# Kernel tuning notes

Hardware: AMD Instinct MI355X
Metric: run time of the kernel (lower is better)

The kernel has to match this reference:

```python
import jax, jax.numpy as jnp
import numpy as np

VOCAB = 32000
EMB = 1024
SEQ = 2048
STACK = 8
N_HEADS = 16
ATTN = 64
BATCH = 2


def _ln(x, g, b, eps=1e-5):
    mu = jnp.mean(x, axis=-1, keepdims=True)
    var = jnp.var(x, axis=-1, keepdims=True)
    return (x - mu) * jax.lax.rsqrt(var + eps) * g + b


def setup_inputs() -> dict:
    key = jax.random.key(0)
    ks = jax.random.split(key, 16)
    s = lambda *sh: 0.02
    inp = {
        "x": jax.random.randint(ks[0], (BATCH, SEQ), 0, VOCAB),
        "emb": jax.random.normal(ks[1], (VOCAB, EMB), jnp.float32) * 0.02,
        # NOTE: one shared Attention_Head (all n_heads identical) and one shared Decoder (all stack layers identical)
        "Wq": jax.random.normal(ks[2], (EMB, ATTN), jnp.float32) * 0.02,
        "bq": jnp.zeros((ATTN,), jnp.float32),
        "Wk": jax.random.normal(ks[3], (EMB, ATTN), jnp.float32) * 0.02,
        "bk": jnp.zeros((ATTN,), jnp.float32),
        "Wv": jax.random.normal(ks[4], (EMB, ATTN), jnp.float32) * 0.02,
        "bv": jnp.zeros((ATTN,), jnp.float32),
        "Wd": jax.random.normal(ks[5], (ATTN * N_HEADS, EMB), jnp.float32) * 0.02,
        "bd": jnp.zeros((EMB,), jnp.float32),
        "g1": jnp.ones((EMB,), jnp.float32),
        "beta1": jnp.zeros((EMB,), jnp.float32),
        "g2": jnp.ones((EMB,), jnp.float32),
        "beta2": jnp.zeros((EMB,), jnp.float32),
        "W1": jax.random.normal(ks[6], (EMB, 4 * EMB), jnp.float32) * 0.02,
        "c1": jnp.zeros((4 * EMB,), jnp.float32),
        "W2": jax.random.normal(ks[7], (4 * EMB, EMB), jnp.float32) * 0.02,
        "c2": jnp.zeros((EMB,), jnp.float32),
        "Wfc": jax.random.normal(ks[8], (EMB, VOCAB), jnp.float32) * 0.02,
        "bfc": jnp.zeros((VOCAB,), jnp.float32),
    }
    return inp


def reference(x, emb, Wq, bq, Wk, bk, Wv, bv, Wd, bd, g1, beta1, g2, beta2, W1, c1, W2, c2, Wfc, bfc):
    h = emb[x]  # [B, S, E]
    scale = ATTN ** (-0.5)
    for _ in range(STACK):  # same (shared) decoder params every layer
        z = _ln(h, g1, beta1)
        q = z @ Wq + bq  # [B,S,A]
        k = z @ Wk + bk
        v = z @ Wv + bv
        # no causal mask applied in the original (tril buffer is unused)
        attn = jax.nn.softmax(jnp.einsum("bqa,bka->bqk", q, k) * scale, axis=-1)
        head = attn @ v  # [B,S,A]; all heads share weights -> identical outputs
        cat = jnp.tile(head, (1, 1, N_HEADS))  # [B,S,A*H]
        h = h + cat @ Wd + bd
        z2 = _ln(h, g2, beta2)
        h = h + jax.nn.relu(z2 @ W1 + c1) @ W2 + c2
    return h @ Wfc + bfc  # [B,S,VOCAB]
```

## Files before the change

kernel.cpp:

```cpp
#include <hip/hip_runtime.h>

typedef unsigned short u16;
typedef __attribute__((ext_vector_type(4))) float f32x4;
typedef __attribute__((ext_vector_type(8))) __bf16 bf16x8;
typedef __attribute__((ext_vector_type(4))) unsigned short u16x4;

static __device__ __forceinline__ u16 f2bf(float f) {
  union { float f; unsigned u; } v; v.f = f;
  unsigned r = v.u + 0x7fffu + ((v.u >> 16) & 1u);
  return (u16)(r >> 16);
}

#define GLD_LDS(g, l) __builtin_amdgcn_global_load_lds( \
    (const __attribute__((address_space(1))) void*)(g), \
    (__attribute__((address_space(3))) void*)(l), 16, 0, 0)

template<int EPI>
__global__ __launch_bounds__(512, 2)
void gemm8p(const u16* __restrict__ A, const u16* __restrict__ B,
            float* __restrict__ Cf, u16* __restrict__ Cb,
            const float* __restrict__ bias, float alpha,
            int K, int lda, int ldb, int ldc, int mtiles, int gm, int nsplit,
            long long sA, long long sB, long long sC)
{
  extern __shared__ u16 lds8[];
  const int t = threadIdx.x;
  const int w = t >> 6, l = t & 63;
  const int l15 = l & 15, l16 = l >> 4;
  const int wr = w >> 2, wc = w & 3;

  int wg = blockIdx.x;
  const int nwg = gridDim.x;
  {
    const int q = nwg >> 3, r = nwg & 7;
    const int xcd = wg & 7, loc = wg >> 3;
    wg = (xcd < r ? xcd * (q + 1) : r * (q + 1) + (xcd - r) * q) + loc;
  }
  const int ntiles = nwg / mtiles;
  const int gsz = gm * ntiles;
  const int gi = wg / gsz;
  const int rr = wg - gi * gsz;
  const int nt = rr / gm;
  const int mt = gi * gm + (rr - nt * gm);
  const int m0 = mt << 8, n0 = nt << 8;

  const int bz = blockIdx.z;
  int batch = bz, sp = 0;
  if (nsplit > 1) { batch = bz / nsplit; sp = bz - batch * nsplit; }
  const u16* Ab = A + (long long)batch * sA + (long long)sp * K;
  const u16* Bb = B + (long long)batch * sB + (long long)sp * K;
  const long long cbase = (long long)bz * sC;

  const int srow = t >> 3;
  const int scol = (((t & 7) ^ (srow & 7)) << 3);
  const u16* gA[4]; const u16* gB[4];
#pragma unroll
  for (int i = 0; i < 4; ++i) {
    gA[i] = Ab + (long long)(m0 + i * 64 + srow) * lda + scol;
    gB[i] = Bb + (long long)(n0 + i * 64 + srow) * ldb + scol;
  }
  const int ldst = w << 9;

  auto STAGE = [&](int buf) {
#pragma unroll
    for (int i = 0; i < 4; ++i) {
      GLD_LDS(gA[i], &lds8[buf * 16384 + i * 4096 + ldst]);
      gA[i] += 64;
    }
#pragma unroll
    for (int i = 0; i < 4; ++i) {
      GLD_LDS(gB[i], &lds8[32768 + buf * 16384 + i * 4096 + ldst]);
      gB[i] += 64;
    }
  };

  STAGE(0);
  STAGE(1);

  f32x4 acc[8][4] = {};
  const int nkt = K >> 6;
  const int aRow = wr * 128 + l15;
  const int bRow = wc * 64 + l15;
  const int swz = l15 & 7;

  for (int kt = 0; kt < nkt; ++kt) {
    const int buf = kt & 1;
    if (kt < nkt - 1) asm volatile("s_waitcnt vmcnt(8)" ::: "memory");
    else              asm volatile("s_waitcnt vmcnt(0)" ::: "memory");
    __builtin_amdgcn_s_barrier();
    __builtin_amdgcn_sched_barrier(0);

    const int abase = buf * 16384;
    const int bbase = 32768 + buf * 16384;
    bf16x8 af[4][2], bf[4][2];
#pragma unroll
    for (int mf = 0; mf < 4; ++mf)
#pragma unroll
      for (int kk = 0; kk < 2; ++kk)
        af[mf][kk] = *(const bf16x8*)&lds8[abase + (aRow + mf * 16) * 64 + ((((kk << 2) + l16)) ^ swz) * 8];
#pragma unroll
    for (int nf = 0; nf < 4; ++nf)
#pragma unroll
      for (int kk = 0; kk < 2; ++kk)
        bf[nf][kk] = *(const bf16x8*)&lds8[bbase + (bRow + nf * 16) * 64 + ((((kk << 2) + l16)) ^ swz) * 8];

    __builtin_amdgcn_s_setprio(1);
#pragma unroll
    for (int mf = 0; mf < 4; ++mf)
#pragma unroll
      for (int nf = 0; nf < 4; ++nf)
#pragma unroll
        for (int kk = 0; kk < 2; ++kk)
          acc[mf][nf] = __builtin_amdgcn_mfma_f32_16x16x32_bf16(af[mf][kk], bf[nf][kk], acc[mf][nf], 0, 0, 0);
    __builtin_amdgcn_s_setprio(0);

    bf16x8 ah[4][2];
#pragma unroll
    for (int mf = 0; mf < 4; ++mf)
#pragma unroll
      for (int kk = 0; kk < 2; ++kk)
        ah[mf][kk] = *(const bf16x8*)&lds8[abase + (aRow + 64 + mf * 16) * 64 + ((((kk << 2) + l16)) ^ swz) * 8];

    asm volatile("s_waitcnt lgkmcnt(0)" ::: "memory");
    __builtin_amdgcn_s_barrier();
    __builtin_amdgcn_sched_barrier(0);
    if (kt + 2 < nkt) STAGE(buf);

    __builtin_amdgcn_s_setprio(1);
#pragma unroll
    for (int mf = 0; mf < 4; ++mf)
#pragma unroll
      for (int nf = 0; nf < 4; ++nf)
#pragma unroll
        for (int kk = 0; kk < 2; ++kk)
          acc[mf + 4][nf] = __builtin_amdgcn_mfma_f32_16x16x32_bf16(ah[mf][kk], bf[nf][kk], acc[mf + 4][nf], 0, 0, 0);
    __builtin_amdgcn_s_setprio(0);
  }

#pragma unroll
  for (int mf = 0; mf < 8; ++mf) {
    const int rbase = m0 + wr * 128 + mf * 16 + l16 * 4;
#pragma unroll
    for (int nf = 0; nf < 4; ++nf) {
      const int col = n0 + wc * 64 + nf * 16 + l15;
      const float bv = bias ? bias[col] : 0.f;
#pragma unroll
      for (int r = 0; r < 4; ++r) {
        const long long idx = cbase + (long long)(rbase + r) * ldc + col;
        const float v = acc[mf][nf][r];
        if (EPI == 0)      Cf[idx] = alpha * v + bv;
        else if (EPI == 2) Cb[idx] = f2bf(v + bv);
        else               { float x = v + bv; Cb[idx] = f2bf(x > 0.f ? x : 0.f); }
      }
    }
  }
}

template<int EPI>
__global__ __launch_bounds__(256)
void gemm_bt(const u16* __restrict__ A, const u16* __restrict__ B,
             float* __restrict__ Cf, u16* __restrict__ Cb,
             const float* __restrict__ bias, float alpha,
             int K, int lda, int ldb, int ldc, int mtiles, int gm, int nsplit,
             long long sA, long long sB, long long sC)
{
  __shared__ u16 ldsA[128 * 32];
  __shared__ u16 ldsB[128 * 32];
  const int t = threadIdx.x;
  const int w = t >> 6, l = t & 63;

  int wg = blockIdx.x;
  const int nwg = gridDim.x;
  {
    const int q = nwg >> 3, r = nwg & 7;
    const int xcd = wg & 7, loc = wg >> 3;
    wg = (xcd < r ? xcd * (q + 1) : r * (q + 1) + (xcd - r) * q) + loc;
  }
  const int ntiles = nwg / mtiles;
  const int gsz = gm * ntiles;
  const int gi = wg / gsz;
  const int rr = wg - gi * gsz;
  const int nt = rr / gm;
  const int mt = gi * gm + (rr - nt * gm);
  const int m0 = mt << 7, n0 = nt << 7;

  const int bzRaw = blockIdx.z;
  int batch = bzRaw, sp = 0;
  if (nsplit > 1) { batch = bzRaw / nsplit; sp = bzRaw - batch * nsplit; }
  const u16* Ab = A + (long long)batch * sA + (long long)sp * K;
  const u16* Bb = B + (long long)batch * sB + (long long)sp * K;
  const long long cbase = (long long)bzRaw * sC;

  const int wr = (w >> 1) << 6, wc = (w & 1) << 6;
  const int l15 = l & 15, l16 = l >> 4;
  f32x4 acc[4][4] = {};

  for (int k0 = 0; k0 < K; k0 += 32) {
#pragma unroll
    for (int r = 0; r < 2; ++r) {
      const int o = (r << 12) + (t << 4);
      const int row = o >> 6;
      const int cole = (o & 63) >> 1;
      GLD_LDS(Ab + (long long)(m0 + row) * lda + k0 + cole, &ldsA[(r << 11) + (w << 9)]);
      GLD_LDS(Bb + (long long)(n0 + row) * ldb + k0 + cole, &ldsB[(r << 11) + (w << 9)]);
    }
    __syncthreads();
    bf16x8 af[4], bg[4];
#pragma unroll
    for (int i = 0; i < 4; ++i) {
      af[i] = *(const bf16x8*)&ldsA[(wr + i * 16 + l15) * 32 + l16 * 8];
      bg[i] = *(const bf16x8*)&ldsB[(wc + i * 16 + l15) * 32 + l16 * 8];
    }
#pragma unroll
    for (int i = 0; i < 4; ++i)
#pragma unroll
      for (int j = 0; j < 4; ++j)
        acc[i][j] = __builtin_amdgcn_mfma_f32_16x16x32_bf16(af[i], bg[j], acc[i][j], 0, 0, 0);
    __syncthreads();
  }

#pragma unroll
  for (int i = 0; i < 4; ++i) {
    const int rbase = m0 + wr + i * 16 + l16 * 4;
#pragma unroll
    for (int j = 0; j < 4; ++j) {
      const int col = n0 + wc + j * 16 + l15;
      const float bv = bias ? bias[col] : 0.f;
#pragma unroll
      for (int r = 0; r < 4; ++r) {
        const long long idx = cbase + (long long)(rbase + r) * ldc + col;
        const float v = acc[i][j][r];
        if (EPI == 0)      Cf[idx] = alpha * v + bv;
        else if (EPI == 1) Cf[idx] += v + bv;
        else if (EPI == 2) Cb[idx] = f2bf(v + bv);
        else               { float x = v + bv; Cb[idx] = f2bf(x > 0.f ? x : 0.f); }
      }
    }
  }
}

__device__ __forceinline__ void fstep(
    const bf16x8 (&ck)[4][2], const bf16x8 (&cv)[4][2],
    bf16x8 (&nk)[4][2], bf16x8 (&nv)[4][2],
    const bf16x8 (&qf)[2], float (&m)[4], float (&ls)[4], f32x4 (&o)[4],
    const u16* qb, const u16* vb, int kv0, int kvn, u16* pl, int l15, int l16)
{
  f32x4 s[4] = {};
#pragma unroll
  for (int ni = 0; ni < 4; ++ni)
#pragma unroll
    for (int kk = 0; kk < 2; ++kk)
      s[ni] = __builtin_amdgcn_mfma_f32_16x16x32_bf16(qf[kk], ck[ni][kk], s[ni], 0, 0, 0);
#pragma unroll
  for (int ni = 0; ni < 4; ++ni)
#pragma unroll
    for (int kk = 0; kk < 2; ++kk)
      nk[ni][kk] = *(const bf16x8*)(qb + (kvn + ni * 16 + l15) * 256 + 64 + kk * 32 + l16 * 8);
#pragma unroll
  for (int ni = 0; ni < 4; ++ni) s[ni] *= 0.125f;
  float al[4], ps[4];
#pragma unroll
  for (int r = 0; r < 4; ++r) {
    float v = fmaxf(fmaxf(s[0][r], s[1][r]), fmaxf(s[2][r], s[3][r]));
    v = fmaxf(v, __shfl_xor(v, 1)); v = fmaxf(v, __shfl_xor(v, 2));
    v = fmaxf(v, __shfl_xor(v, 4)); v = fmaxf(v, __shfl_xor(v, 8));
    const float mn = fmaxf(m[r], v);
    al[r] = __expf(m[r] - mn);
    m[r] = mn;
    ps[r] = 0.f;
  }
#pragma unroll
  for (int ni = 0; ni < 4; ++ni)
#pragma unroll
    for (int r = 0; r < 4; ++r) {
      const float p = __expf(s[ni][r] - m[r]);
      ps[r] += p;
      pl[(l16 * 4 + r) * 72 + ni * 16 + l15] = f2bf(p);
    }
#pragma unroll
  for (int r = 0; r < 4; ++r) {
    float t = ps[r];
    t += __shfl_xor(t, 1); t += __shfl_xor(t, 2);
    t += __shfl_xor(t, 4); t += __shfl_xor(t, 8);
    ls[r] = ls[r] * al[r] + t;
  }
#pragma unroll
  for (int nd = 0; nd < 4; ++nd)
#pragma unroll
    for (int r = 0; r < 4; ++r) o[nd][r] *= al[r];
  bf16x8 pa[2];
#pragma unroll
  for (int kk = 0; kk < 2; ++kk)
    pa[kk] = *(const bf16x8*)&pl[l15 * 72 + kk * 32 + l16 * 8];
#pragma unroll
  for (int nd = 0; nd < 4; ++nd)
#pragma unroll
    for (int kk = 0; kk < 2; ++kk)
      o[nd] = __builtin_amdgcn_mfma_f32_16x16x32_bf16(pa[kk], cv[nd][kk], o[nd], 0, 0, 0);
#pragma unroll
  for (int nd = 0; nd < 4; ++nd)
#pragma unroll
    for (int kk = 0; kk < 2; ++kk)
      nv[nd][kk] = *(const bf16x8*)(vb + (nd * 16 + l15) * 2048 + kvn + kk * 32 + l16 * 8);
  (void)kv0;
}

__global__ __launch_bounds__(64)
void flash_k(const u16* __restrict__ qkv, const u16* __restrict__ vT,
             u16* __restrict__ head)
{
  __shared__ u16 pl[16 * 72];
  const int l = threadIdx.x, l15 = l & 15, l16 = l >> 4;
  const int b = blockIdx.x >> 7, q0 = (blockIdx.x & 127) << 4;
  const u16* qb = qkv + (long long)b * 2048 * 256;
  const u16* vb = vT + (long long)b * 64 * 2048;
  bf16x8 qf[2];
#pragma unroll
  for (int kk = 0; kk < 2; ++kk)
    qf[kk] = *(const bf16x8*)(qb + (q0 + l15) * 256 + kk * 32 + l16 * 8);
  float m[4], ls[4];
  f32x4 o[4] = {};
#pragma unroll
  for (int r = 0; r < 4; ++r) { m[r] = -1e30f; ls[r] = 0.f; }
  bf16x8 ka[4][2], va[4][2], kb[4][2], vb2[4][2];
#pragma unroll
  for (int ni = 0; ni < 4; ++ni)
#pragma unroll
    for (int kk = 0; kk < 2; ++kk) {
      ka[ni][kk] = *(const bf16x8*)(qb + (ni * 16 + l15) * 256 + 64 + kk * 32 + l16 * 8);
      va[ni][kk] = *(const bf16x8*)(vb + (ni * 16 + l15) * 2048 + kk * 32 + l16 * 8);
    }
  for (int t = 0; t < 32; t += 2) {
    fstep(ka, va, kb, vb2, qf, m, ls, o, qb, vb, t * 64, (t + 1) * 64, pl, l15, l16);
    fstep(kb, vb2, ka, va, qf, m, ls, o, qb, vb, (t + 1) * 64,
          (t + 2 < 32 ? (t + 2) * 64 : 31 * 64), pl, l15, l16);
  }
#pragma unroll
  for (int nd = 0; nd < 4; ++nd)
#pragma unroll
    for (int r = 0; r < 4; ++r)
      head[((long long)b * 2048 + q0 + l16 * 4 + r) * 64 + nd * 16 + l15] =
          f2bf(o[nd][r] / ls[r]);
}

__global__ __launch_bounds__(256)
void ln_k(const float* __restrict__ x, const float* __restrict__ g,
          const float* __restrict__ b, u16* __restrict__ z)
{
  const long long row = blockIdx.x;
  f32x4 v = ((const f32x4*)(x + row * 1024))[threadIdx.x];
  float s = v[0] + v[1] + v[2] + v[3];
  float q = v[0] * v[0] + v[1] * v[1] + v[2] * v[2] + v[3] * v[3];
#pragma unroll
  for (int o = 32; o; o >>= 1) { s += __shfl_down(s, o); q += __shfl_down(q, o); }
  __shared__ float rs_[4], rq_[4];
  const int l = threadIdx.x & 63, w = threadIdx.x >> 6;
  if (l == 0) { rs_[w] = s; rq_[w] = q; }
  __syncthreads();
  s = rs_[0] + rs_[1] + rs_[2] + rs_[3];
  q = rq_[0] + rq_[1] + rq_[2] + rq_[3];
  const float mu = s * (1.f / 1024.f);
  const float rstd = rsqrtf(q * (1.f / 1024.f) - mu * mu + 1e-5f);
  const f32x4 gv = ((const f32x4*)g)[threadIdx.x];
  const f32x4 bv = ((const f32x4*)b)[threadIdx.x];
  u16x4 o4;
#pragma unroll
  for (int e = 0; e < 4; ++e) o4[e] = f2bf((v[e] - mu) * rstd * gv[e] + bv[e]);
  ((u16x4*)(z + row * 1024))[threadIdx.x] = o4;
}

template<int MODE>
__global__ __launch_bounds__(256)
void reduce_ln_k(const u16* __restrict__ p, float* __restrict__ h,
                 const float* __restrict__ c2, const float* __restrict__ g,
                 const float* __restrict__ b, u16* __restrict__ z)
{
  const long long row = blockIdx.x;
  const int t = threadIdx.x;
  const long long i4 = (row << 8) + t;
  f32x4 v = ((const f32x4*)h)[i4] + ((const f32x4*)c2)[t];
#pragma unroll
  for (int s = 0; s < 4; ++s) {
    u16x4 pv = ((const u16x4*)p)[i4 + (long long)s * 1048576];
#pragma unroll
    for (int e = 0; e < 4; ++e) {
      union { unsigned u; float f; } x; x.u = ((unsigned)pv[e]) << 16;
      v[e] += x.f;
    }
  }
  u16x4 o4;
  if (MODE == 1) {
#pragma unroll
    for (int e = 0; e < 4; ++e) o4[e] = f2bf(v[e]);
  } else {
    ((f32x4*)h)[i4] = v;
    float s = v[0] + v[1] + v[2] + v[3];
    float q = v[0] * v[0] + v[1] * v[1] + v[2] * v[2] + v[3] * v[3];
#pragma unroll
    for (int o = 32; o; o >>= 1) { s += __shfl_down(s, o); q += __shfl_down(q, o); }
    __shared__ float rs_[4], rq_[4];
    const int l = t & 63, w = t >> 6;
    if (l == 0) { rs_[w] = s; rq_[w] = q; }
    __syncthreads();
    s = rs_[0] + rs_[1] + rs_[2] + rs_[3];
    q = rq_[0] + rq_[1] + rq_[2] + rq_[3];
    const float mu = s * (1.f / 1024.f);
    const float rstd = rsqrtf(q * (1.f / 1024.f) - mu * mu + 1e-5f);
    const f32x4 gv = ((const f32x4*)g)[t];
    const f32x4 bv = ((const f32x4*)b)[t];
#pragma unroll
    for (int e = 0; e < 4; ++e) o4[e] = f2bf((v[e] - mu) * rstd * gv[e] + bv[e]);
  }
  ((u16x4*)z)[i4] = o4;
}

__global__ __launch_bounds__(256)
void gather_k(const int* __restrict__ x, const float* __restrict__ emb, float* __restrict__ h)
{
  const long long tok = blockIdx.x;
  const long long r = (long long)x[tok] << 8;
  ((f32x4*)h)[(tok << 8) + threadIdx.x] = ((const f32x4*)emb)[r + threadIdx.x];
}

__global__ __launch_bounds__(256)
void tcast_k(const float* __restrict__ in, u16* __restrict__ out, int R, int C)
{
  __shared__ float tile[32][33];
  const int tx = threadIdx.x & 31, ty = threadIdx.x >> 5;
  const long long r0 = (long long)blockIdx.y << 5, c0 = (long long)blockIdx.x << 5;
#pragma unroll
  for (int yy = 0; yy < 32; yy += 8)
    tile[ty + yy][tx] = in[(r0 + ty + yy) * C + c0 + tx];
  __syncthreads();
#pragma unroll
  for (int yy = 0; yy < 32; yy += 8)
    out[(c0 + ty + yy) * R + r0 + tx] = f2bf(tile[tx][ty + yy]);
}

__global__ __launch_bounds__(256)
void wqkv_k(const float* __restrict__ Wq, const float* __restrict__ Wk,
            const float* __restrict__ Wv, u16* __restrict__ o)
{
  const int n = blockIdx.y;
  const long long e = (long long)blockIdx.x * 256 + threadIdx.x;
  float v = 0.f;
  if (n < 64)       v = Wq[e * 64 + n];
  else if (n < 128) v = Wk[e * 64 + (n - 64)];
  else if (n < 192) v = Wv[e * 64 + (n - 128)];
  o[(long long)n * 1024 + e] = f2bf(v);
}

__global__ __launch_bounds__(256)
void bqkv_k(const float* __restrict__ bq, const float* __restrict__ bk,
            const float* __restrict__ bv, float* __restrict__ o)
{
  const int n = threadIdx.x;
  float v = 0.f;
  if (n < 64)       v = bq[n];
  else if (n < 128) v = bk[n - 64];
  else if (n < 192) v = bv[n - 128];
  o[n] = v;
}

__global__ __launch_bounds__(256)
void wdsum_k(const float* __restrict__ Wd, u16* __restrict__ o)
{
  const int i = blockIdx.x * 256 + threadIdx.x;
  const int a = i & 63, e = i >> 6;
  float s = 0.f;
#pragma unroll
  for (int hh = 0; hh < 16; ++hh) s += Wd[(long long)(hh * 64 + a) * 1024 + e];
  o[i] = f2bf(s);
}

__global__ __launch_bounds__(256)
void reduce_qkv(const float* __restrict__ p, const float* __restrict__ bqkv,
                u16* __restrict__ qkv, u16* __restrict__ vT)
{
  const long long i4 = (long long)blockIdx.x * 256 + threadIdx.x;
  const int c4 = (int)(i4 & 63);
  const long long row = i4 >> 6;
  f32x4 s = ((const f32x4*)p)[i4] + ((const f32x4*)p)[i4 + 262144]
          + ((const f32x4*)bqkv)[c4];
  u16x4 o;
#pragma unroll
  for (int e = 0; e < 4; ++e) o[e] = f2bf(s[e]);
  ((u16x4*)qkv)[i4] = o;
  if (c4 >= 32 && c4 < 48) {
    const long long b = row >> 11, sidx = row & 2047;
#pragma unroll
    for (int e = 0; e < 4; ++e) {
      const int a = (c4 - 32) * 4 + e;
      vT[(b * 64 + a) * 2048 + sidx] = o[e];
    }
  }
}

extern "C" void kernel_launch(void* const* d_in, const int* in_sizes, int n_in,
                              void* d_out, int out_size, void* d_ws, size_t ws_size,
                              hipStream_t stream) {
  const int*   x   = (const int*)d_in[0];
  const float* emb = (const float*)d_in[1];
  const float* Wq  = (const float*)d_in[2];
  const float* bq  = (const float*)d_in[3];
  const float* Wk  = (const float*)d_in[4];
  const float* bk  = (const float*)d_in[5];
  const float* Wv  = (const float*)d_in[6];
  const float* bv  = (const float*)d_in[7];
  const float* Wd  = (const float*)d_in[8];
  const float* bd  = (const float*)d_in[9];
  const float* g1  = (const float*)d_in[10];
  const float* be1 = (const float*)d_in[11];
  const float* g2  = (const float*)d_in[12];
  const float* be2 = (const float*)d_in[13];
  const float* W1  = (const float*)d_in[14];
  const float* c1  = (const float*)d_in[15];
  const float* W2  = (const float*)d_in[16];
  const float* c2  = (const float*)d_in[17];
  const float* Wfc = (const float*)d_in[18];
  const float* bfc = (const float*)d_in[19];
  float* out = (float*)d_out;

  hipFuncSetAttribute(reinterpret_cast<const void*>(gemm8p<0>),
                      hipFuncAttributeMaxDynamicSharedMemorySize, 131072);
  hipFuncSetAttribute(reinterpret_cast<const void*>(gemm8p<2>),
                      hipFuncAttributeMaxDynamicSharedMemorySize, 131072);
  hipFuncSetAttribute(reinterpret_cast<const void*>(gemm8p<3>),
                      hipFuncAttributeMaxDynamicSharedMemorySize, 131072);

  char* ws = (char*)d_ws;
  size_t off = 0;
  auto alloc = [&](size_t bytes) { void* p = ws + off; off = (off + bytes + 255) & ~(size_t)255; return p; };
  float*  h     = (float*) alloc(4096ull * 1024 * 4);
  u16*    z     = (u16*)   alloc(4096ull * 1024 * 2);
  u16*    qkv   = (u16*)   alloc(4096ull * 256 * 2);
  u16*    vT    = (u16*)   alloc(2ull * 64 * 2048 * 2);
  u16*    head  = (u16*)   alloc(4096ull * 64 * 2);
  u16*    mid   = (u16*)   alloc(4096ull * 4096 * 2);
  char*   SCR   = (char*)  alloc(2ull * 4096 * 1024 * 4);
  float*  partQ = (float*)SCR;
  u16*    partF = (u16*)SCR;
  u16*    Wqkvt = (u16*)   alloc(256ull * 1024 * 2);
  float*  bqkv  = (float*) alloc(256 * 4);
  u16*    Wdst  = (u16*)   alloc(1024ull * 64 * 2);
  u16*    W1t   = (u16*)   alloc(4096ull * 1024 * 2);
  u16*    W2t   = (u16*)   alloc(1024ull * 4096 * 2);
  u16*    Wfct  = (u16*)   alloc(32000ull * 1024 * 2);

  gather_k<<<4096, 256, 0, stream>>>(x, emb, h);
  wqkv_k<<<dim3(4, 256), 256, 0, stream>>>(Wq, Wk, Wv, Wqkvt);
  bqkv_k<<<1, 256, 0, stream>>>(bq, bk, bv, bqkv);
  wdsum_k<<<256, 256, 0, stream>>>(Wd, Wdst);
  tcast_k<<<dim3(128, 32), 256, 0, stream>>>(W1, W1t, 1024, 4096);
  tcast_k<<<dim3(32, 128), 256, 0, stream>>>(W2, W2t, 4096, 1024);
  tcast_k<<<dim3(1000, 32), 256, 0, stream>>>(Wfc, Wfct, 1024, 32000);

  for (int layer = 0; layer < 8; ++layer) {
    if (layer == 0)
      ln_k<<<4096, 256, 0, stream>>>(h, g1, be1, z);
    gemm_bt<0><<<dim3(64, 1, 2), 256, 0, stream>>>(z, Wqkvt, partQ, nullptr, nullptr, 1.f,
        512, 1024, 1024, 256, 32, 32, 2, 0, 0, 1048576);
    reduce_qkv<<<1024, 256, 0, stream>>>(partQ, bqkv, qkv, vT);
    flash_k<<<256, 64, 0, stream>>>(qkv, vT, head);
    gemm_bt<1><<<dim3(256, 1, 1), 256, 0, stream>>>(head, Wdst, h, nullptr, bd, 1.f,
        64, 64, 64, 1024, 32, 32, 1, 0, 0, 0);
    ln_k<<<4096, 256, 0, stream>>>(h, g2, be2, z);
    gemm8p<3><<<dim3(256, 1, 1), 512, 131072, stream>>>(z, W1t, nullptr, mid, c1, 1.f,
        1024, 1024, 1024, 4096, 16, 16, 1, 0, 0, 0);
    gemm8p<2><<<dim3(64, 1, 4), 512, 131072, stream>>>(mid, W2t, nullptr, partF, nullptr, 1.f,
        1024, 4096, 4096, 1024, 16, 16, 4, 0, 0, 4194304);
    if (layer < 7)
      reduce_ln_k<0><<<4096, 256, 0, stream>>>(partF, h, c2, g1, be1, z);
    else
      reduce_ln_k<1><<<4096, 256, 0, stream>>>(partF, h, c2, nullptr, nullptr, z);
  }
  gemm8p<0><<<dim3(2000, 1, 1), 512, 131072, stream>>>(z, Wfct, out, nullptr, bfc, 1.f,
      1024, 1024, 1024, 32000, 16, 8, 1, 0, 0, 0);
}
```

Measured before the change: 1.759 ms.

## Restructure GEMM main loop into four interleaved phases with split A/B staging

Rewrites the bf16 MFMA GEMM mainloop so each k-tile is processed in four quarter phases, each reading a subset of A/B fragments from LDS and issuing part of the next tile's global-to-LDS loads between MFMA bursts. A is staged one tile ahead and B two tiles ahead, in half-tile chunks with a new per-thread load layout. The goal is to hide global load latency and LDS reads behind MFMA work more evenly. In exchange it adds more barriers per iteration, which may cost synchronisation overhead.

```diff
diff --git a/kernel.cpp b/kernel.cpp
--- a/kernel.cpp
+++ b/kernel.cpp
@@ -14,6 +14,11 @@
 #define GLD_LDS(g, l) __builtin_amdgcn_global_load_lds( \
     (const __attribute__((address_space(1))) void*)(g), \
     (__attribute__((address_space(3))) void*)(l), 16, 0, 0)
+
+#define LGKM0() asm volatile("s_waitcnt lgkmcnt(0)" ::: "memory")
+#define SBAR() do { __builtin_amdgcn_sched_barrier(0); \
+                    __builtin_amdgcn_s_barrier(); \
+                    __builtin_amdgcn_sched_barrier(0); } while (0)
 
 template<int EPI>
 __global__ __launch_bounds__(512, 2)
@@ -51,91 +56,107 @@
   const u16* Bb = B + (long long)batch * sB + (long long)sp * K;
   const long long cbase = (long long)bz * sC;
 
-  const int srow = t >> 3;
-  const int scol = (((t & 7) ^ (srow & 7)) << 3);
-  const u16* gA[4]; const u16* gB[4];
-#pragma unroll
-  for (int i = 0; i < 4; ++i) {
-    gA[i] = Ab + (long long)(m0 + i * 64 + srow) * lda + scol;
-    gB[i] = Bb + (long long)(n0 + i * 64 + srow) * ldb + scol;
-  }
-  const int ldst = w << 9;
-
-  auto STAGE = [&](int buf) {
-#pragma unroll
-    for (int i = 0; i < 4; ++i) {
-      GLD_LDS(gA[i], &lds8[buf * 16384 + i * 4096 + ldst]);
-      gA[i] += 64;
-    }
-#pragma unroll
-    for (int i = 0; i < 4; ++i) {
-      GLD_LDS(gB[i], &lds8[32768 + buf * 16384 + i * 4096 + ldst]);
-      gB[i] += 64;
-    }
+  int srow[2], scol[2], sdst[2];
+#pragma unroll
+  for (int j = 0; j < 2; ++j) {
+    const int u = (j << 9) + (w << 6) + l;
+    srow[j] = u >> 3;
+    scol[j] = ((u & 7) ^ ((u >> 3) & 7)) << 3;
+    sdst[j] = ((j << 9) + (w << 6)) << 3;
+  }
+
+  auto STAGE_A = [&](int buf, int h, int ktgt) {
+#pragma unroll
+    for (int j = 0; j < 2; ++j)
+      GLD_LDS(Ab + (long long)(m0 + h * 128 + srow[j]) * lda + ktgt * 64 + scol[j],
+              &lds8[(buf * 2 + h) * 8192 + sdst[j]]);
   };
-
-  STAGE(0);
-  STAGE(1);
-
+  auto STAGE_B = [&](int buf, int h, int ktgt) {
+#pragma unroll
+    for (int j = 0; j < 2; ++j)
+      GLD_LDS(Bb + (long long)(n0 + h * 128 + srow[j]) * ldb + ktgt * 64 + scol[j],
+              &lds8[32768 + (buf * 2 + h) * 8192 + sdst[j]]);
+  };
+
+  bf16x8 aF[4][2], bF0[2][2], bF1[2][2];
   f32x4 acc[8][4] = {};
+
+  auto RDA = [&](int buf, int mbase) {
+#pragma unroll
+    for (int mf = 0; mf < 4; ++mf) {
+      const int r2 = (mbase + mf) * 16 + l15;
+#pragma unroll
+      for (int kk = 0; kk < 2; ++kk)
+        aF[mf][kk] = *(const bf16x8*)&lds8[(buf * 2 + wr) * 8192 + r2 * 64 +
+                                           (((kk << 2) + l16) ^ (r2 & 7)) * 8];
+    }
+  };
+  auto RDB = [&](bf16x8 (&dst)[2][2], int buf, int nbase) {
+#pragma unroll
+    for (int nf = 0; nf < 2; ++nf) {
+      const int r2 = (wc & 1) * 64 + (nbase + nf) * 16 + l15;
+#pragma unroll
+      for (int kk = 0; kk < 2; ++kk)
+        dst[nf][kk] = *(const bf16x8*)&lds8[32768 + (buf * 2 + (wc >> 1)) * 8192 + r2 * 64 +
+                                            (((kk << 2) + l16) ^ (r2 & 7)) * 8];
+    }
+  };
+
+#define MM16(MB, NB, BF) \
+  do { \
+    __builtin_amdgcn_s_setprio(1); \
+    _Pragma("unroll") \
+    for (int mf = 0; mf < 4; ++mf) \
+      _Pragma("unroll") \
+      for (int nf = 0; nf < 2; ++nf) \
+        _Pragma("unroll") \
+        for (int kk = 0; kk < 2; ++kk) \
+          acc[MB + mf][NB + nf] = __builtin_amdgcn_mfma_f32_16x16x32_bf16( \
+              aF[mf][kk], BF[nf][kk], acc[MB + mf][NB + nf], 0, 0, 0); \
+    __builtin_amdgcn_s_setprio(0); \
+  } while (0)
+
   const int nkt = K >> 6;
-  const int aRow = wr * 128 + l15;
-  const int bRow = wc * 64 + l15;
-  const int swz = l15 & 7;
+
+  STAGE_B(0, 0, 0); STAGE_B(0, 1, 0);
+  STAGE_A(0, 0, 0); STAGE_A(0, 1, 0);
+  if (1 < nkt) { STAGE_B(1, 0, 1); STAGE_B(1, 1, 1); }
+  asm volatile("s_waitcnt vmcnt(4)" ::: "memory");
+  SBAR();
 
   for (int kt = 0; kt < nkt; ++kt) {
-    const int buf = kt & 1;
-    if (kt < nkt - 1) asm volatile("s_waitcnt vmcnt(8)" ::: "memory");
-    else              asm volatile("s_waitcnt vmcnt(0)" ::: "memory");
-    __builtin_amdgcn_s_barrier();
+    const int buf = kt & 1, nb = buf ^ 1;
+    RDA(buf, 0); RDB(bF0, buf, 0);
+    if (kt + 1 < nkt) STAGE_A(nb, 0, kt + 1);
+    SBAR();
+    LGKM0();
     __builtin_amdgcn_sched_barrier(0);
-
-    const int abase = buf * 16384;
-    const int bbase = 32768 + buf * 16384;
-    bf16x8 af[4][2], bf[4][2];
-#pragma unroll
-    for (int mf = 0; mf < 4; ++mf)
-#pragma unroll
-      for (int kk = 0; kk < 2; ++kk)
-        af[mf][kk] = *(const bf16x8*)&lds8[abase + (aRow + mf * 16) * 64 + ((((kk << 2) + l16)) ^ swz) * 8];
-#pragma unroll
-    for (int nf = 0; nf < 4; ++nf)
-#pragma unroll
-      for (int kk = 0; kk < 2; ++kk)
-        bf[nf][kk] = *(const bf16x8*)&lds8[bbase + (bRow + nf * 16) * 64 + ((((kk << 2) + l16)) ^ swz) * 8];
-
-    __builtin_amdgcn_s_setprio(1);
-#pragma unroll
-    for (int mf = 0; mf < 4; ++mf)
-#pragma unroll
-      for (int nf = 0; nf < 4; ++nf)
-#pragma unroll
-        for (int kk = 0; kk < 2; ++kk)
-          acc[mf][nf] = __builtin_amdgcn_mfma_f32_16x16x32_bf16(af[mf][kk], bf[nf][kk], acc[mf][nf], 0, 0, 0);
-    __builtin_amdgcn_s_setprio(0);
-
-    bf16x8 ah[4][2];
-#pragma unroll
-    for (int mf = 0; mf < 4; ++mf)
-#pragma unroll
-      for (int kk = 0; kk < 2; ++kk)
-        ah[mf][kk] = *(const bf16x8*)&lds8[abase + (aRow + 64 + mf * 16) * 64 + ((((kk << 2) + l16)) ^ swz) * 8];
-
-    asm volatile("s_waitcnt lgkmcnt(0)" ::: "memory");
-    __builtin_amdgcn_s_barrier();
+    MM16(0, 0, bF0);
+    SBAR();
+    RDB(bF1, buf, 2);
+    if (kt + 1 < nkt) STAGE_A(nb, 1, kt + 1);
+    SBAR();
+    LGKM0();
     __builtin_amdgcn_sched_barrier(0);
-    if (kt + 2 < nkt) STAGE(buf);
-
-    __builtin_amdgcn_s_setprio(1);
-#pragma unroll
-    for (int mf = 0; mf < 4; ++mf)
-#pragma unroll
-      for (int nf = 0; nf < 4; ++nf)
-#pragma unroll
-        for (int kk = 0; kk < 2; ++kk)
-          acc[mf + 4][nf] = __builtin_amdgcn_mfma_f32_16x16x32_bf16(ah[mf][kk], bf[nf][kk], acc[mf + 4][nf], 0, 0, 0);
-    __builtin_amdgcn_s_setprio(0);
-  }
+    MM16(0, 2, bF1);
+    SBAR();
+    RDA(buf, 4);
+    if (kt + 2 < nkt) STAGE_B(buf, 0, kt + 2);
+    SBAR();
+    LGKM0();
+    __builtin_amdgcn_sched_barrier(0);
+    MM16(4, 0, bF0);
+    SBAR();
+    if (kt + 2 < nkt) STAGE_B(buf, 1, kt + 2);
+    SBAR();
+    MM16(4, 2, bF1);
+    if (kt + 1 < nkt) {
+      if (kt + 2 < nkt) asm volatile("s_waitcnt vmcnt(4)" ::: "memory");
+      else              asm volatile("s_waitcnt vmcnt(0)" ::: "memory");
+    }
+    SBAR();
+  }
+#undef MM16
 
 #pragma unroll
   for (int mf = 0; mf < 8; ++mf) {
```

Result: no change. 1.794 ms (+2.0%).

## Replace 256x256 eight-wave GEMM with 128x128 four-wave kernel using static LDS

Applied to the files above, without the earlier changes.

Swaps the large-tile 512-thread GEMM (256x256 tiles, K-step 64, 128KB dynamic LDS) for a 256-thread kernel with 128x128 tiles, K-step 32 and 32KB of static LDS, with occupancy raised to three blocks per CU. The FFN and final vocab projections now launch four times as many workgroups. The aim is more workgroups and better latency hiding and load balance across CUs. In exchange each tile reuses less data, so global/L2 traffic per FLOP rises, and the LDS swizzle and sync pattern change.

```diff
diff --git a/kernel.cpp b/kernel.cpp
--- a/kernel.cpp
+++ b/kernel.cpp
@@ -15,19 +15,24 @@
     (const __attribute__((address_space(1))) void*)(g), \
     (__attribute__((address_space(3))) void*)(l), 16, 0, 0)
 
+#define LGKM0() asm volatile("s_waitcnt lgkmcnt(0)" ::: "memory")
+#define SBAR() do { __builtin_amdgcn_sched_barrier(0); \
+                    __builtin_amdgcn_s_barrier(); \
+                    __builtin_amdgcn_sched_barrier(0); } while (0)
+
 template<int EPI>
-__global__ __launch_bounds__(512, 2)
-void gemm8p(const u16* __restrict__ A, const u16* __restrict__ B,
+__global__ __launch_bounds__(256, 3)
+void gemm4w(const u16* __restrict__ A, const u16* __restrict__ B,
             float* __restrict__ Cf, u16* __restrict__ Cb,
             const float* __restrict__ bias, float alpha,
             int K, int lda, int ldb, int ldc, int mtiles, int gm, int nsplit,
             long long sA, long long sB, long long sC)
 {
-  extern __shared__ u16 lds8[];
+  __shared__ u16 lds[16384];
   const int t = threadIdx.x;
   const int w = t >> 6, l = t & 63;
   const int l15 = l & 15, l16 = l >> 4;
-  const int wr = w >> 2, wc = w & 3;
+  const int wr = w >> 1, wc = w & 1;
 
   int wg = blockIdx.x;
   const int nwg = gridDim.x;
@@ -42,104 +47,71 @@
   const int rr = wg - gi * gsz;
   const int nt = rr / gm;
   const int mt = gi * gm + (rr - nt * gm);
-  const int m0 = mt << 8, n0 = nt << 8;
+  const int m0 = mt << 7, n0 = nt << 7;
 
   const int bz = blockIdx.z;
   int batch = bz, sp = 0;
   if (nsplit > 1) { batch = bz / nsplit; sp = bz - batch * nsplit; }
-  const u16* Ab = A + (long long)batch * sA + (long long)sp * K;
-  const u16* Bb = B + (long long)batch * sB + (long long)sp * K;
+  const u16* Ab = A + (long long)batch * sA + (long long)sp * K + m0 * (long long)lda;
+  const u16* Bb = B + (long long)batch * sB + (long long)sp * K + n0 * (long long)ldb;
   const long long cbase = (long long)bz * sC;
 
-  const int srow = t >> 3;
-  const int scol = (((t & 7) ^ (srow & 7)) << 3);
-  const u16* gA[4]; const u16* gB[4];
-#pragma unroll
-  for (int i = 0; i < 4; ++i) {
-    gA[i] = Ab + (long long)(m0 + i * 64 + srow) * lda + scol;
-    gB[i] = Bb + (long long)(n0 + i * 64 + srow) * ldb + scol;
-  }
-  const int ldst = w << 9;
-
+  const u16* pa[2]; const u16* pb[2];
+  int sdst[2];
+#pragma unroll
+  for (int j = 0; j < 2; ++j) {
+    const int u = w * 128 + j * 64 + l;
+    const int row = u >> 2;
+    const int sl = (u & 3) ^ ((row >> 1) & 3);
+    sdst[j] = (w * 128 + j * 64) * 8;
+    pa[j] = Ab + (long long)row * lda + sl * 8;
+    pb[j] = Bb + (long long)row * ldb + sl * 8;
+  }
   auto STAGE = [&](int buf) {
 #pragma unroll
-    for (int i = 0; i < 4; ++i) {
-      GLD_LDS(gA[i], &lds8[buf * 16384 + i * 4096 + ldst]);
-      gA[i] += 64;
-    }
-#pragma unroll
-    for (int i = 0; i < 4; ++i) {
-      GLD_LDS(gB[i], &lds8[32768 + buf * 16384 + i * 4096 + ldst]);
-      gB[i] += 64;
-    }
+    for (int j = 0; j < 2; ++j) { GLD_LDS(pa[j], &lds[buf * 8192 + sdst[j]]); pa[j] += 32; }
+#pragma unroll
+    for (int j = 0; j < 2; ++j) { GLD_LDS(pb[j], &lds[buf * 8192 + 4096 + sdst[j]]); pb[j] += 32; }
   };
 
+  const int nkt = K >> 5;
   STAGE(0);
-  STAGE(1);
-
-  f32x4 acc[8][4] = {};
-  const int nkt = K >> 6;
-  const int aRow = wr * 128 + l15;
-  const int bRow = wc * 64 + l15;
-  const int swz = l15 & 7;
+  if (nkt > 1) STAGE(1);
+
+  f32x4 acc[4][4] = {};
 
   for (int kt = 0; kt < nkt; ++kt) {
     const int buf = kt & 1;
-    if (kt < nkt - 1) asm volatile("s_waitcnt vmcnt(8)" ::: "memory");
+    if (kt + 1 < nkt) asm volatile("s_waitcnt vmcnt(4)" ::: "memory");
     else              asm volatile("s_waitcnt vmcnt(0)" ::: "memory");
-    __builtin_amdgcn_s_barrier();
+    SBAR();
+    bf16x8 af[4], bg[4];
+#pragma unroll
+    for (int mf = 0; mf < 4; ++mf) {
+      const int r2 = wr * 64 + mf * 16 + l15;
+      af[mf] = *(const bf16x8*)&lds[buf * 8192 + r2 * 32 + (l16 ^ ((r2 >> 1) & 3)) * 8];
+    }
+#pragma unroll
+    for (int nf = 0; nf < 4; ++nf) {
+      const int r2 = wc * 64 + nf * 16 + l15;
+      bg[nf] = *(const bf16x8*)&lds[buf * 8192 + 4096 + r2 * 32 + (l16 ^ ((r2 >> 1) & 3)) * 8];
+    }
+    LGKM0();
     __builtin_amdgcn_sched_barrier(0);
-
-    const int abase = buf * 16384;
-    const int bbase = 32768 + buf * 16384;
-    bf16x8 af[4][2], bf[4][2];
+    SBAR();
+    if (kt + 2 < nkt) STAGE(buf);
+    __builtin_amdgcn_s_setprio(1);
 #pragma unroll
     for (int mf = 0; mf < 4; ++mf)
 #pragma unroll
-      for (int kk = 0; kk < 2; ++kk)
-        af[mf][kk] = *(const bf16x8*)&lds8[abase + (aRow + mf * 16) * 64 + ((((kk << 2) + l16)) ^ swz) * 8];
-#pragma unroll
-    for (int nf = 0; nf < 4; ++nf)
-#pragma unroll
-      for (int kk = 0; kk < 2; ++kk)
-        bf[nf][kk] = *(const bf16x8*)&lds8[bbase + (bRow + nf * 16) * 64 + ((((kk << 2) + l16)) ^ swz) * 8];
-
-    __builtin_amdgcn_s_setprio(1);
-#pragma unroll
-    for (int mf = 0; mf < 4; ++mf)
-#pragma unroll
       for (int nf = 0; nf < 4; ++nf)
-#pragma unroll
-        for (int kk = 0; kk < 2; ++kk)
-          acc[mf][nf] = __builtin_amdgcn_mfma_f32_16x16x32_bf16(af[mf][kk], bf[nf][kk], acc[mf][nf], 0, 0, 0);
+        acc[mf][nf] = __builtin_amdgcn_mfma_f32_16x16x32_bf16(af[mf], bg[nf], acc[mf][nf], 0, 0, 0);
     __builtin_amdgcn_s_setprio(0);
-
-    bf16x8 ah[4][2];
-#pragma unroll
-    for (int mf = 0; mf < 4; ++mf)
-#pragma unroll
-      for (int kk = 0; kk < 2; ++kk)
-        ah[mf][kk] = *(const bf16x8*)&lds8[abase + (aRow + 64 + mf * 16) * 64 + ((((kk << 2) + l16)) ^ swz) * 8];
-
-    asm volatile("s_waitcnt lgkmcnt(0)" ::: "memory");
-    __builtin_amdgcn_s_barrier();
-    __builtin_amdgcn_sched_barrier(0);
-    if (kt + 2 < nkt) STAGE(buf);
-
-    __builtin_amdgcn_s_setprio(1);
-#pragma unroll
-    for (int mf = 0; mf < 4; ++mf)
-#pragma unroll
-      for (int nf = 0; nf < 4; ++nf)
-#pragma unroll
-        for (int kk = 0; kk < 2; ++kk)
-          acc[mf + 4][nf] = __builtin_amdgcn_mfma_f32_16x16x32_bf16(ah[mf][kk], bf[nf][kk], acc[mf + 4][nf], 0, 0, 0);
-    __builtin_amdgcn_s_setprio(0);
-  }
-
-#pragma unroll
-  for (int mf = 0; mf < 8; ++mf) {
-    const int rbase = m0 + wr * 128 + mf * 16 + l16 * 4;
+  }
+
+#pragma unroll
+  for (int mf = 0; mf < 4; ++mf) {
+    const int rbase = m0 + wr * 64 + mf * 16 + l16 * 4;
 #pragma unroll
     for (int nf = 0; nf < 4; ++nf) {
       const int col = n0 + wc * 64 + nf * 16 + l15;
@@ -521,13 +493,6 @@
   const float* bfc = (const float*)d_in[19];
   float* out = (float*)d_out;
 
-  hipFuncSetAttribute(reinterpret_cast<const void*>(gemm8p<0>),
-                      hipFuncAttributeMaxDynamicSharedMemorySize, 131072);
-  hipFuncSetAttribute(reinterpret_cast<const void*>(gemm8p<2>),
-                      hipFuncAttributeMaxDynamicSharedMemorySize, 131072);
-  hipFuncSetAttribute(reinterpret_cast<const void*>(gemm8p<3>),
-                      hipFuncAttributeMaxDynamicSharedMemorySize, 131072);
-
   char* ws = (char*)d_ws;
   size_t off = 0;
   auto alloc = [&](size_t bytes) { void* p = ws + off; off = (off + bytes + 255) & ~(size_t)255; return p; };
@@ -565,15 +530,15 @@
     gemm_bt<1><<<dim3(256, 1, 1), 256, 0, stream>>>(head, Wdst, h, nullptr, bd, 1.f,
         64, 64, 64, 1024, 32, 32, 1, 0, 0, 0);
     ln_k<<<4096, 256, 0, stream>>>(h, g2, be2, z);
-    gemm8p<3><<<dim3(256, 1, 1), 512, 131072, stream>>>(z, W1t, nullptr, mid, c1, 1.f,
-        1024, 1024, 1024, 4096, 16, 16, 1, 0, 0, 0);
-    gemm8p<2><<<dim3(64, 1, 4), 512, 131072, stream>>>(mid, W2t, nullptr, partF, nullptr, 1.f,
-        1024, 4096, 4096, 1024, 16, 16, 4, 0, 0, 4194304);
+    gemm4w<3><<<dim3(1024, 1, 1), 256, 0, stream>>>(z, W1t, nullptr, mid, c1, 1.f,
+        1024, 1024, 1024, 4096, 32, 16, 1, 0, 0, 0);
+    gemm4w<2><<<dim3(256, 1, 4), 256, 0, stream>>>(mid, W2t, nullptr, partF, nullptr, 1.f,
+        1024, 4096, 4096, 1024, 32, 16, 4, 0, 0, 4194304);
     if (layer < 7)
       reduce_ln_k<0><<<4096, 256, 0, stream>>>(partF, h, c2, g1, be1, z);
     else
       reduce_ln_k<1><<<4096, 256, 0, stream>>>(partF, h, c2, nullptr, nullptr, z);
   }
-  gemm8p<0><<<dim3(2000, 1, 1), 512, 131072, stream>>>(z, Wfct, out, nullptr, bfc, 1.f,
-      1024, 1024, 1024, 32000, 16, 8, 1, 0, 0, 0);
-}
+  gemm4w<0><<<dim3(8000, 1, 1), 256, 0, stream>>>(z, Wfct, out, nullptr, bfc, 1.f,
+      1024, 1024, 1024, 32000, 32, 16, 1, 0, 0, 0);
+}
```

Measured after the change: 1.954 ms. 11.1% more time.

## Split attention KV range four ways with separate merge kernel

Applied to the files above, without the earlier changes.

The flash attention kernel now splits the 2048-key range into four chunks, so 1024 single-wave blocks run instead of 256. Each block writes its unnormalized partial output plus running max and sum to scratch. A new merge kernel combines the four partials with log-sum-exp rescaling and writes the bf16 head. The aim is to fill more compute units on a GPU that was underused by 256 single-wave blocks, at the cost of an extra launch and a round trip of partials through memory.

```diff
diff --git a/kernel.cpp b/kernel.cpp
--- a/kernel.cpp
+++ b/kernel.cpp
@@ -243,7 +243,7 @@
     const bf16x8 (&ck)[4][2], const bf16x8 (&cv)[4][2],
     bf16x8 (&nk)[4][2], bf16x8 (&nv)[4][2],
     const bf16x8 (&qf)[2], float (&m)[4], float (&ls)[4], f32x4 (&o)[4],
-    const u16* qb, const u16* vb, int kv0, int kvn, u16* pl, int l15, int l16)
+    const u16* qb, const u16* vb, int kvn, u16* pl, int l15, int l16)
 {
   f32x4 s[4] = {};
 #pragma unroll
@@ -302,16 +302,17 @@
 #pragma unroll
     for (int kk = 0; kk < 2; ++kk)
       nv[nd][kk] = *(const bf16x8*)(vb + (nd * 16 + l15) * 2048 + kvn + kk * 32 + l16 * 8);
-  (void)kv0;
 }
 
 __global__ __launch_bounds__(64)
-void flash_k(const u16* __restrict__ qkv, const u16* __restrict__ vT,
-             u16* __restrict__ head)
+void flashp_k(const u16* __restrict__ qkv, const u16* __restrict__ vT,
+              float* __restrict__ po, float* __restrict__ pm, float* __restrict__ pls)
 {
   __shared__ u16 pl[16 * 72];
   const int l = threadIdx.x, l15 = l & 15, l16 = l >> 4;
-  const int b = blockIdx.x >> 7, q0 = (blockIdx.x & 127) << 4;
+  const int idx = blockIdx.x;
+  const int b = idx >> 9, rest = idx & 511, sp = rest >> 7, qt = rest & 127;
+  const int q0 = qt << 4, kvb = sp << 9;
   const u16* qb = qkv + (long long)b * 2048 * 256;
   const u16* vb = vT + (long long)b * 64 * 2048;
   bf16x8 qf[2];
@@ -327,20 +328,51 @@
   for (int ni = 0; ni < 4; ++ni)
 #pragma unroll
     for (int kk = 0; kk < 2; ++kk) {
-      ka[ni][kk] = *(const bf16x8*)(qb + (ni * 16 + l15) * 256 + 64 + kk * 32 + l16 * 8);
-      va[ni][kk] = *(const bf16x8*)(vb + (ni * 16 + l15) * 2048 + kk * 32 + l16 * 8);
-    }
-  for (int t = 0; t < 32; t += 2) {
-    fstep(ka, va, kb, vb2, qf, m, ls, o, qb, vb, t * 64, (t + 1) * 64, pl, l15, l16);
-    fstep(kb, vb2, ka, va, qf, m, ls, o, qb, vb, (t + 1) * 64,
-          (t + 2 < 32 ? (t + 2) * 64 : 31 * 64), pl, l15, l16);
-  }
+      ka[ni][kk] = *(const bf16x8*)(qb + (kvb + ni * 16 + l15) * 256 + 64 + kk * 32 + l16 * 8);
+      va[ni][kk] = *(const bf16x8*)(vb + (ni * 16 + l15) * 2048 + kvb + kk * 32 + l16 * 8);
+    }
+  for (int ti = 0; ti < 8; ti += 2) {
+    const int n1 = kvb + (ti + 1 < 8 ? (ti + 1) * 64 : 7 * 64);
+    const int n2 = kvb + (ti + 2 < 8 ? (ti + 2) * 64 : 7 * 64);
+    fstep(ka, va, kb, vb2, qf, m, ls, o, qb, vb, n1, pl, l15, l16);
+    fstep(kb, vb2, ka, va, qf, m, ls, o, qb, vb, n2, pl, l15, l16);
+  }
+  const long long pidx = ((long long)(b * 128 + qt)) * 4 + sp;
 #pragma unroll
   for (int nd = 0; nd < 4; ++nd)
 #pragma unroll
     for (int r = 0; r < 4; ++r)
-      head[((long long)b * 2048 + q0 + l16 * 4 + r) * 64 + nd * 16 + l15] =
-          f2bf(o[nd][r] / ls[r]);
+      po[pidx * 1024 + (l16 * 4 + r) * 64 + nd * 16 + l15] = o[nd][r];
+  if (l15 == 0) {
+#pragma unroll
+    for (int r = 0; r < 4; ++r) {
+      pm[pidx * 16 + l16 * 4 + r] = m[r];
+      pls[pidx * 16 + l16 * 4 + r] = ls[r];
+    }
+  }
+}
+
+__global__ __launch_bounds__(64)
+void fmerge_k(const float* __restrict__ po, const float* __restrict__ pm,
+              const float* __restrict__ pls, u16* __restrict__ head)
+{
+  const int idx = blockIdx.x;
+  const int d = threadIdx.x;
+  const long long base = (long long)idx * 4;
+#pragma unroll
+  for (int r = 0; r < 16; ++r) {
+    float M = -1e30f;
+#pragma unroll
+    for (int sp = 0; sp < 4; ++sp) M = fmaxf(M, pm[(base + sp) * 16 + r]);
+    float L = 0.f, acc = 0.f;
+#pragma unroll
+    for (int sp = 0; sp < 4; ++sp) {
+      const float e = __expf(pm[(base + sp) * 16 + r] - M);
+      L += pls[(base + sp) * 16 + r] * e;
+      acc += po[(base + sp) * 1024 + r * 64 + d] * e;
+    }
+    head[((long long)idx * 16 + r) * 64 + d] = f2bf(acc / L);
+  }
 }
 
 __global__ __launch_bounds__(256)
@@ -539,6 +571,9 @@
   u16*    mid   = (u16*)   alloc(4096ull * 4096 * 2);
   char*   SCR   = (char*)  alloc(2ull * 4096 * 1024 * 4);
   float*  partQ = (float*)SCR;
+  float*  po    = (float*)SCR;
+  float*  pm    = (float*)(SCR + 4194304);
+  float*  pls   = (float*)(SCR + 4194304 + 65536);
   u16*    partF = (u16*)SCR;
   u16*    Wqkvt = (u16*)   alloc(256ull * 1024 * 2);
   float*  bqkv  = (float*) alloc(256 * 4);
@@ -561,7 +596,8 @@
     gemm_bt<0><<<dim3(64, 1, 2), 256, 0, stream>>>(z, Wqkvt, partQ, nullptr, nullptr, 1.f,
         512, 1024, 1024, 256, 32, 32, 2, 0, 0, 1048576);
     reduce_qkv<<<1024, 256, 0, stream>>>(partQ, bqkv, qkv, vT);
-    flash_k<<<256, 64, 0, stream>>>(qkv, vT, head);
+    flashp_k<<<1024, 64, 0, stream>>>(qkv, vT, po, pm, pls);
+    fmerge_k<<<256, 64, 0, stream>>>(po, pm, pls, head);
     gemm_bt<1><<<dim3(256, 1, 1), 256, 0, stream>>>(head, Wdst, h, nullptr, bd, 1.f,
         64, 64, 64, 1024, 32, 32, 1, 0, 0, 0);
     ln_k<<<4096, 256, 0, stream>>>(h, g2, be2, z);
```

Result: slower. 1.807 ms (+2.7%).
